# Kernel optimization log

Hardware: AMD Instinct MI355X
Metric: run time of the kernel (lower is better)

The kernel has to match this reference:

```python
import jax, jax.numpy as jnp
import numpy as np

N = 65536          # total nodes
B = 64             # graphs in batch
NPG = N // B       # nodes per graph (equal-size graphs)
K = 128            # n_clusters (assignment dim)
D_IN = 128         # node feature dim
D = 128            # pooled feature dim
E = 1048576        # edges (avg degree 16)


def setup_inputs() -> dict:
    key = jax.random.key(0)
    k1, k2, k3, k4, k5, k6 = jax.random.split(key, 6)
    h = jax.random.normal(k1, (N, D_IN), dtype=jnp.float32)
    fea = jax.random.normal(k2, (B * K, D), dtype=jnp.float32)
    W_self = jax.random.normal(k3, (D_IN, K), dtype=jnp.float32) / np.sqrt(D_IN)
    W_neigh = jax.random.normal(k4, (D_IN, K), dtype=jnp.float32) / np.sqrt(D_IN)
    b = jnp.zeros((K,), dtype=jnp.float32)
    # edges kept within each graph: sample local ids then offset by graph base
    base = jnp.repeat(jnp.arange(B, dtype=jnp.int64) * NPG, E // B)
    edge_src = jax.random.randint(k5, (E,), 0, NPG, dtype=jnp.int64) + base
    edge_dst = jax.random.randint(k6, (E,), 0, NPG, dtype=jnp.int64) + base
    return {"h": h, "fea": fea, "W_self": W_self, "W_neigh": W_neigh,
            "b": b, "edge_src": edge_src, "edge_dst": edge_dst}


def reference(h, fea, W_self, W_neigh, b, edge_src, edge_dst):
    # GraphSage mean aggregation: neigh[i] = mean_{j: (j->i)} h[j]
    deg = jnp.zeros((N,), h.dtype).at[edge_dst].add(1.0)
    neigh = jnp.zeros((N, D_IN), h.dtype).at[edge_dst].add(h[edge_src])
    neigh = neigh / jnp.maximum(deg, 1.0)[:, None]
    assign = jax.nn.relu(h @ W_self + neigh @ W_neigh + b)       # [N, K]
    assign = jax.nn.softmax(assign, axis=1)                       # softmax over clusters
    # block-diagonal mm == per-graph GEMM: [B, n, K] @ [B, K, D] -> [B, n, D]
    out = jnp.einsum('bnk,bkd->bnd',
                     assign.reshape(B, NPG, K),
                     fea.reshape(B, K, D))
    return out.reshape(N, D)
```

## Files before the change

### kernel.cpp

```cpp
#include <hip/hip_runtime.h>

#define N_NODES 65536
#define B_G     64
#define NPG     1024
#define KC      128
#define DIN     128
#define E_EDGES 1048576
#define EPG     16384
#define CSTRIDE (EPG + NPG)

typedef __attribute__((ext_vector_type(8))) short short8;
typedef __attribute__((ext_vector_type(4))) float floatx4;

static __device__ __forceinline__ short f2bf(float x) {
    unsigned u = __float_as_uint(x);
    unsigned r = (u + 0x7FFF + ((u >> 16) & 1)) >> 16;
    return (short)r;
}
static __device__ __forceinline__ unsigned pack2(float a, float b) {
    return (unsigned)(unsigned short)f2bf(a) | ((unsigned)(unsigned short)f2bf(b) << 16);
}

__global__ __launch_bounds__(256) void setup_kernel(
    const float* __restrict__ Wself, const float* __restrict__ Wneigh,
    const float* __restrict__ fea, const float* __restrict__ h,
    const int* __restrict__ esrc, const int* __restrict__ edst,
    short* __restrict__ wt, short* __restrict__ feaT, short* __restrict__ h_bf,
    unsigned short* __restrict__ csr, int* __restrict__ offs, int* __restrict__ deg)
{
    int bid = blockIdx.x;
    int tid = threadIdx.x;
    if (bid < B_G) {
        __shared__ int cnt[NPG];
        __shared__ int ofl[NPG];
        __shared__ int ssc[256];
        int g = bid;
        int gbase = g * NPG;
        for (int i = tid; i < NPG; i += 256) cnt[i] = 0;
        __syncthreads();
        const int* ed = edst + (size_t)g * EPG;
        const int* es = esrc + (size_t)g * EPG;
        for (int it = 0; it < EPG / 256; it++)
            atomicAdd(&cnt[ed[it * 256 + tid] - gbase], 1);
        __syncthreads();
        int b[4], p[4];
        int lsum = 0;
#pragma unroll
        for (int i = 0; i < 4; i++) {
            b[i] = cnt[4 * tid + i];
            p[i] = (b[i] + 1) & ~1;
            lsum += p[i];
        }
        ssc[tid] = lsum;
        __syncthreads();
        for (int off = 1; off < 256; off <<= 1) {
            int v = ssc[tid];
            int vv = (tid >= off) ? ssc[tid - off] : 0;
            __syncthreads();
            ssc[tid] = v + vv;
            __syncthreads();
        }
        int base = ssc[tid] - lsum;
#pragma unroll
        for (int i = 0; i < 4; i++) {
            ofl[4 * tid + i] = base;
            offs[gbase + 4 * tid + i] = base;
            deg[gbase + 4 * tid + i] = b[i];
            base += p[i];
        }
        __syncthreads();
        unsigned short* cg = csr + (size_t)g * CSTRIDE;
        for (int it = 0; it < EPG / 256; it++) {
            int e = it * 256 + tid;
            int d = ed[e] - gbase;
            int s = es[e] - gbase;
            int pos = atomicAdd(&ofl[d], 1);
            cg[pos] = (unsigned short)s;
        }
    } else {
        long idx = (long)(bid - B_G) * 256 + tid;
        if (idx < 32768) {
            int n = (int)(idx >> 8), k = (int)(idx & 255);
            float v = (k < 128) ? Wself[k * 128 + n] : Wneigh[(k - 128) * 128 + n];
            wt[idx] = f2bf(v);
        } else if (idx < 32768 + 1048576) {
            long fi = idx - 32768;
            int g = (int)(fi >> 14), d = (int)((fi >> 7) & 127), k = (int)(fi & 127);
            feaT[fi] = f2bf(fea[((long)g * 128 + k) * 128 + d]);
        } else {
            long gi = idx - 32768 - 1048576;
            const float4* hp = (const float4*)h + gi * 2;
            float4 a = hp[0], b4 = hp[1];
            uint4 w;
            w.x = pack2(a.x, a.y);
            w.y = pack2(a.z, a.w);
            w.z = pack2(b4.x, b4.y);
            w.w = pack2(b4.z, b4.w);
            ((uint4*)h_bf)[gi] = w;
        }
    }
}

__global__ __launch_bounds__(256) void agg_kernel(
    const short* __restrict__ h_bf, const unsigned short* __restrict__ csr,
    const int* __restrict__ offs, const int* __restrict__ deg,
    short* __restrict__ neigh)
{
    int g = blockIdx.x & 63;
    int chunk = blockIdx.x >> 6;
    int wave = threadIdx.x >> 6, lane = threadIdx.x & 63;
    int local = chunk * 4 + wave;
    int node = g * NPG + local;
    int start = offs[node];
    int m = deg[node];
    const unsigned short* lst = csr + (size_t)g * CSTRIDE + start;
    const uint2* rows = (const uint2*)h_bf + (size_t)g * NPG * 32;
    int l31 = lane & 31;
    int hi = lane >> 5;
    float s0 = 0.f, s1 = 0.f, s2 = 0.f, s3 = 0.f;
    int pairs = m >> 1;
    int p = 0;
    for (; p + 4 <= pairs; p += 4) {
        unsigned pp[4];
#pragma unroll
        for (int u = 0; u < 4; u++) pp[u] = *(const unsigned*)(lst + 2 * (p + u));
        uint2 v[4];
#pragma unroll
        for (int u = 0; u < 4; u++) {
            int s = hi ? (int)(pp[u] >> 16) : (int)(pp[u] & 0xffff);
            v[u] = rows[s * 32 + l31];
        }
#pragma unroll
        for (int u = 0; u < 4; u++) {
            s0 += __uint_as_float(v[u].x << 16);
            s1 += __uint_as_float(v[u].x & 0xffff0000u);
            s2 += __uint_as_float(v[u].y << 16);
            s3 += __uint_as_float(v[u].y & 0xffff0000u);
        }
    }
    for (; p < pairs; p++) {
        unsigned pp = *(const unsigned*)(lst + 2 * p);
        int s = hi ? (int)(pp >> 16) : (int)(pp & 0xffff);
        uint2 vv = rows[s * 32 + l31];
        s0 += __uint_as_float(vv.x << 16);
        s1 += __uint_as_float(vv.x & 0xffff0000u);
        s2 += __uint_as_float(vv.y << 16);
        s3 += __uint_as_float(vv.y & 0xffff0000u);
    }
    if (m & 1) {
        int s = lst[m - 1];
        if (!hi) {
            uint2 vv = rows[s * 32 + l31];
            s0 += __uint_as_float(vv.x << 16);
            s1 += __uint_as_float(vv.x & 0xffff0000u);
            s2 += __uint_as_float(vv.y << 16);
            s3 += __uint_as_float(vv.y & 0xffff0000u);
        }
    }
    s0 += __shfl_xor(s0, 32, 64);
    s1 += __shfl_xor(s1, 32, 64);
    s2 += __shfl_xor(s2, 32, 64);
    s3 += __shfl_xor(s3, 32, 64);
    if (!hi) {
        float invd = 1.0f / fmaxf((float)m, 1.0f);
        uint2 w;
        w.x = pack2(s0 * invd, s1 * invd);
        w.y = pack2(s2 * invd, s3 * invd);
        ((uint2*)neigh)[(size_t)node * 32 + l31] = w;
    }
}

__global__ __launch_bounds__(256) void fused_kernel(
    const short* __restrict__ h_bf, const short* __restrict__ neigh,
    const short* __restrict__ wt, const float* __restrict__ bias,
    const short* __restrict__ feaT, float* __restrict__ out)
{
    __shared__ __align__(16) char smem[50688];
    short* lds_a = (short*)smem;
    short* lds_b = lds_a + 128 * 72;
    short* ldsP  = (short*)smem;
    short* ldsB2 = ldsP + 128 * 132;

    int tid = threadIdx.x;
    int tile_m = blockIdx.x * 128;
    int g = tile_m >> 10;
    int wave = tid >> 6, lane = tid & 63;
    int l15 = lane & 15, quad = lane >> 4;

    floatx4 zz = {0.f, 0.f, 0.f, 0.f};
    floatx4 acc[2][8];
#pragma unroll
    for (int i = 0; i < 2; i++)
#pragma unroll
        for (int j = 0; j < 8; j++) acc[i][j] = zz;

    int row_s = tid >> 1;
    int c0 = (tid & 1) * 32;

    for (int kk = 0; kk < 4; kk++) {
        const short* src = (kk < 2)
            ? h_bf + (size_t)(tile_m + row_s) * DIN + kk * 64 + c0
            : neigh + (size_t)(tile_m + row_s) * DIN + (kk - 2) * 64 + c0;
        short* dsta = lds_a + row_s * 72 + c0;
#pragma unroll
        for (int i = 0; i < 32; i += 8)
            *reinterpret_cast<short8*>(dsta + i) = *reinterpret_cast<const short8*>(src + i);
        const short* srcb = wt + row_s * 256 + kk * 64 + c0;
        short* dstb = lds_b + row_s * 72 + c0;
#pragma unroll
        for (int i = 0; i < 32; i += 8)
            *reinterpret_cast<short8*>(dstb + i) = *reinterpret_cast<const short8*>(srcb + i);
        __syncthreads();
#pragma unroll
        for (int ks = 0; ks < 2; ks++) {
            short8 af[2];
#pragma unroll
            for (int rb = 0; rb < 2; rb++) {
                int m = wave * 32 + rb * 16 + l15;
                af[rb] = *reinterpret_cast<const short8*>(lds_a + m * 72 + ks * 32 + quad * 8);
            }
#pragma unroll
            for (int cb = 0; cb < 8; cb++) {
                int n = cb * 16 + l15;
                short8 bf = *reinterpret_cast<const short8*>(lds_b + n * 72 + ks * 32 + quad * 8);
                acc[0][cb] = __builtin_amdgcn_mfma_f32_16x16x32_bf16(af[0], bf, acc[0][cb], 0, 0, 0);
                acc[1][cb] = __builtin_amdgcn_mfma_f32_16x16x32_bf16(af[1], bf, acc[1][cb], 0, 0, 0);
            }
        }
        __syncthreads();
    }

    float bv[8];
#pragma unroll
    for (int cb = 0; cb < 8; cb++) bv[cb] = bias[cb * 16 + l15];

#pragma unroll
    for (int rb = 0; rb < 2; rb++) {
#pragma unroll
        for (int v = 0; v < 4; v++) {
            float x[8];
            float m = -1e30f;
#pragma unroll
            for (int cb = 0; cb < 8; cb++) {
                float t = acc[rb][cb][v] + bv[cb];
                t = fmaxf(t, 0.f);
                x[cb] = t;
                m = fmaxf(m, t);
            }
#pragma unroll
            for (int off = 1; off < 16; off <<= 1) m = fmaxf(m, __shfl_xor(m, off, 64));
            float s = 0.f;
#pragma unroll
            for (int cb = 0; cb < 8; cb++) { x[cb] = __expf(x[cb] - m); s += x[cb]; }
#pragma unroll
            for (int off = 1; off < 16; off <<= 1) s += __shfl_xor(s, off, 64);
            float inv = 1.0f / s;
            int row = wave * 32 + rb * 16 + quad * 4 + v;
#pragma unroll
            for (int cb = 0; cb < 8; cb++)
                ldsP[row * 132 + cb * 16 + l15] = f2bf(x[cb] * inv);
        }
    }

    floatx4 oacc[2][8];
#pragma unroll
    for (int i = 0; i < 2; i++)
#pragma unroll
        for (int j = 0; j < 8; j++) oacc[i][j] = zz;

    int r2 = tid >> 2;
    int c2 = (tid & 3) * 32;
    short8 pf[2][4];

    for (int half = 0; half < 2; half++) {
        if (half) __syncthreads();
        const short* srcb = feaT + ((size_t)g * 128 + half * 64 + r2) * 128 + c2;
        short* dstb = ldsB2 + r2 * 132 + c2;
#pragma unroll
        for (int i = 0; i < 32; i += 8)
            *reinterpret_cast<short8*>(dstb + i) = *reinterpret_cast<const short8*>(srcb + i);
        __syncthreads();
        if (half == 0) {
#pragma unroll
            for (int rb = 0; rb < 2; rb++)
#pragma unroll
                for (int ks = 0; ks < 4; ks++)
                    pf[rb][ks] = *reinterpret_cast<const short8*>(
                        ldsP + (wave * 32 + rb * 16 + l15) * 132 + ks * 32 + quad * 8);
        }
#pragma unroll
        for (int cb2 = 0; cb2 < 4; cb2++) {
            int cb = half * 4 + cb2;
#pragma unroll
            for (int ks = 0; ks < 4; ks++) {
                short8 bf = *reinterpret_cast<const short8*>(
                    ldsB2 + (cb2 * 16 + l15) * 132 + ks * 32 + quad * 8);
                oacc[0][cb] = __builtin_amdgcn_mfma_f32_16x16x32_bf16(pf[0][ks], bf, oacc[0][cb], 0, 0, 0);
                oacc[1][cb] = __builtin_amdgcn_mfma_f32_16x16x32_bf16(pf[1][ks], bf, oacc[1][cb], 0, 0, 0);
            }
        }
    }

#pragma unroll
    for (int rb = 0; rb < 2; rb++)
#pragma unroll
        for (int v = 0; v < 4; v++) {
            int row = tile_m + wave * 32 + rb * 16 + quad * 4 + v;
#pragma unroll
            for (int cb = 0; cb < 8; cb++)
                out[(size_t)row * 128 + cb * 16 + l15] = oacc[rb][cb][v];
        }
}

extern "C" void kernel_launch(void* const* d_in, const int* in_sizes, int n_in,
                              void* d_out, int out_size, void* d_ws, size_t ws_size,
                              hipStream_t stream) {
    const float* h      = (const float*)d_in[0];
    const float* fea    = (const float*)d_in[1];
    const float* Wself  = (const float*)d_in[2];
    const float* Wneigh = (const float*)d_in[3];
    const float* bias   = (const float*)d_in[4];
    const int*   esrc   = (const int*)d_in[5];
    const int*   edst   = (const int*)d_in[6];
    float* out = (float*)d_out;

    char* ws = (char*)d_ws;
    short* h_bf = (short*)ws;
    size_t off = (size_t)N_NODES * DIN * sizeof(short);
    short* neigh = (short*)(ws + off); off += (size_t)N_NODES * DIN * sizeof(short);
    short* wt    = (short*)(ws + off); off += (size_t)128 * 256 * sizeof(short);
    short* feaT  = (short*)(ws + off); off += (size_t)B_G * 128 * 128 * sizeof(short);
    unsigned short* csr = (unsigned short*)(ws + off); off += (size_t)B_G * CSTRIDE * sizeof(short);
    int* offs = (int*)(ws + off); off += (size_t)N_NODES * sizeof(int);
    int* deg  = (int*)(ws + off);

    setup_kernel<<<64 + 8320, 256, 0, stream>>>(Wself, Wneigh, fea, h, esrc, edst,
                                                wt, feaT, h_bf, csr, offs, deg);
    agg_kernel<<<256 * B_G, 256, 0, stream>>>(h_bf, csr, offs, deg, neigh);
    fused_kernel<<<N_NODES / 128, 256, 0, stream>>>(h_bf, neigh, wt, bias, feaT, out);
}
```

Baseline: 188.2 us.

## Split per-graph CSR build into sliced count, scan and scatter kernels

The single per-graph CSR construction block (64 blocks, each serially processing 16K edges) is replaced by three kernels. Eight slices per graph count degrees in parallel, a 1024-thread block per graph scans the counts and computes per-slice offsets, and eight blocks per graph scatter the source ids. This spreads the serial edge work across far more blocks to improve GPU occupancy during setup. It adds two kernel launches and extra global traffic for the slice count and offset arrays.

Measured after the change: 175.6 us. 1.07x faster.

```diff
diff --git a/kernel.cpp b/kernel.cpp
--- a/kernel.cpp
+++ b/kernel.cpp
@@ -7,6 +7,8 @@
 #define DIN     128
 #define E_EDGES 1048576
 #define EPG     16384
+#define NSLICE  8
+#define SLICE_E (EPG / NSLICE)
 #define CSTRIDE (EPG + NPG)
 
 typedef __attribute__((ext_vector_type(8))) short short8;
@@ -21,64 +23,30 @@
     return (unsigned)(unsigned short)f2bf(a) | ((unsigned)(unsigned short)f2bf(b) << 16);
 }
 
-__global__ __launch_bounds__(256) void setup_kernel(
+__global__ __launch_bounds__(256) void setup_a(
     const float* __restrict__ Wself, const float* __restrict__ Wneigh,
     const float* __restrict__ fea, const float* __restrict__ h,
-    const int* __restrict__ esrc, const int* __restrict__ edst,
+    const int* __restrict__ edst,
     short* __restrict__ wt, short* __restrict__ feaT, short* __restrict__ h_bf,
-    unsigned short* __restrict__ csr, int* __restrict__ offs, int* __restrict__ deg)
+    int* __restrict__ slicecnt)
 {
     int bid = blockIdx.x;
     int tid = threadIdx.x;
-    if (bid < B_G) {
+    if (bid < B_G * NSLICE) {
         __shared__ int cnt[NPG];
-        __shared__ int ofl[NPG];
-        __shared__ int ssc[256];
-        int g = bid;
-        int gbase = g * NPG;
+        int g = bid >> 3, s = bid & 7;
+        int gbase = g << 10;
         for (int i = tid; i < NPG; i += 256) cnt[i] = 0;
         __syncthreads();
-        const int* ed = edst + (size_t)g * EPG;
-        const int* es = esrc + (size_t)g * EPG;
-        for (int it = 0; it < EPG / 256; it++)
+        const int* ed = edst + (size_t)g * EPG + s * SLICE_E;
+#pragma unroll
+        for (int it = 0; it < SLICE_E / 256; it++)
             atomicAdd(&cnt[ed[it * 256 + tid] - gbase], 1);
         __syncthreads();
-        int b[4], p[4];
-        int lsum = 0;
-#pragma unroll
-        for (int i = 0; i < 4; i++) {
-            b[i] = cnt[4 * tid + i];
-            p[i] = (b[i] + 1) & ~1;
-            lsum += p[i];
-        }
-        ssc[tid] = lsum;
-        __syncthreads();
-        for (int off = 1; off < 256; off <<= 1) {
-            int v = ssc[tid];
-            int vv = (tid >= off) ? ssc[tid - off] : 0;
-            __syncthreads();
-            ssc[tid] = v + vv;
-            __syncthreads();
-        }
-        int base = ssc[tid] - lsum;
-#pragma unroll
-        for (int i = 0; i < 4; i++) {
-            ofl[4 * tid + i] = base;
-            offs[gbase + 4 * tid + i] = base;
-            deg[gbase + 4 * tid + i] = b[i];
-            base += p[i];
-        }
-        __syncthreads();
-        unsigned short* cg = csr + (size_t)g * CSTRIDE;
-        for (int it = 0; it < EPG / 256; it++) {
-            int e = it * 256 + tid;
-            int d = ed[e] - gbase;
-            int s = es[e] - gbase;
-            int pos = atomicAdd(&ofl[d], 1);
-            cg[pos] = (unsigned short)s;
-        }
+        int* sc = slicecnt + ((size_t)bid << 10);
+        for (int i = tid; i < NPG; i += 256) sc[i] = cnt[i];
     } else {
-        long idx = (long)(bid - B_G) * 256 + tid;
+        long idx = (long)(bid - B_G * NSLICE) * 256 + tid;
         if (idx < 32768) {
             int n = (int)(idx >> 8), k = (int)(idx & 255);
             float v = (k < 128) ? Wself[k * 128 + n] : Wneigh[(k - 128) * 128 + n];
@@ -101,6 +69,66 @@
     }
 }
 
+__global__ __launch_bounds__(1024) void setup_b(
+    const int* __restrict__ slicecnt, int* __restrict__ offs,
+    int* __restrict__ deg, int* __restrict__ sliceoffs)
+{
+    __shared__ int sa[NPG];
+    int g = blockIdx.x;
+    int tid = threadIdx.x;
+    int s8[NSLICE];
+    int d = 0;
+#pragma unroll
+    for (int s = 0; s < NSLICE; s++) {
+        s8[s] = slicecnt[(((size_t)g * NSLICE + s) << 10) + tid];
+        d += s8[s];
+    }
+    int p = (d + 1) & ~1;
+    sa[tid] = p;
+    __syncthreads();
+    for (int off = 1; off < NPG; off <<= 1) {
+        int v = sa[tid];
+        int vv = (tid >= off) ? sa[tid - off] : 0;
+        __syncthreads();
+        sa[tid] = v + vv;
+        __syncthreads();
+    }
+    int excl = sa[tid] - p;
+    offs[(g << 10) + tid] = excl;
+    deg[(g << 10) + tid] = d;
+    int run = excl;
+#pragma unroll
+    for (int s = 0; s < NSLICE; s++) {
+        sliceoffs[(((size_t)g * NSLICE + s) << 10) + tid] = run;
+        run += s8[s];
+    }
+}
+
+__global__ __launch_bounds__(256) void setup_c(
+    const int* __restrict__ esrc, const int* __restrict__ edst,
+    const int* __restrict__ sliceoffs, unsigned short* __restrict__ csr)
+{
+    __shared__ int cur[NPG];
+    int bid = blockIdx.x;
+    int tid = threadIdx.x;
+    int g = bid >> 3, s = bid & 7;
+    int gbase = g << 10;
+    const int* so = sliceoffs + ((size_t)bid << 10);
+    for (int i = tid; i < NPG; i += 256) cur[i] = so[i];
+    __syncthreads();
+    const int* ed = edst + (size_t)g * EPG + s * SLICE_E;
+    const int* es = esrc + (size_t)g * EPG + s * SLICE_E;
+    unsigned short* cg = csr + (size_t)g * CSTRIDE;
+#pragma unroll
+    for (int it = 0; it < SLICE_E / 256; it++) {
+        int e = it * 256 + tid;
+        int d = ed[e] - gbase;
+        int src = es[e] - gbase;
+        int pos = atomicAdd(&cur[d], 1);
+        cg[pos] = (unsigned short)src;
+    }
+}
+
 __global__ __launch_bounds__(256) void agg_kernel(
     const short* __restrict__ h_bf, const unsigned short* __restrict__ csr,
     const int* __restrict__ offs, const int* __restrict__ deg,
@@ -332,10 +360,14 @@
     short* feaT  = (short*)(ws + off); off += (size_t)B_G * 128 * 128 * sizeof(short);
     unsigned short* csr = (unsigned short*)(ws + off); off += (size_t)B_G * CSTRIDE * sizeof(short);
     int* offs = (int*)(ws + off); off += (size_t)N_NODES * sizeof(int);
-    int* deg  = (int*)(ws + off);
-
-    setup_kernel<<<64 + 8320, 256, 0, stream>>>(Wself, Wneigh, fea, h, esrc, edst,
-                                                wt, feaT, h_bf, csr, offs, deg);
+    int* deg  = (int*)(ws + off); off += (size_t)N_NODES * sizeof(int);
+    int* slicecnt  = (int*)(ws + off); off += (size_t)B_G * NSLICE * NPG * sizeof(int);
+    int* sliceoffs = (int*)(ws + off);
+
+    setup_a<<<B_G * NSLICE + 8320, 256, 0, stream>>>(Wself, Wneigh, fea, h, edst,
+                                                     wt, feaT, h_bf, slicecnt);
+    setup_b<<<B_G, 1024, 0, stream>>>(slicecnt, offs, deg, sliceoffs);
+    setup_c<<<B_G * NSLICE, 256, 0, stream>>>(esrc, edst, sliceoffs, csr);
     agg_kernel<<<256 * B_G, 256, 0, stream>>>(h_bf, csr, offs, deg, neigh);
     fused_kernel<<<N_NODES / 128, 256, 0, stream>>>(h_bf, neigh, wt, bias, feaT, out);
 }
```
